# Performance work log

Measured on AMD Instinct MI355X. Metric: run time of the kernel, lower is better.

Reference implementation:

```python
import jax, jax.numpy as jnp
import numpy as np
from jax.scipy.special import logsumexp

ENTROPY_REG = 0.1   # entropy regularization (temperature)
N_ITERS = 100       # Sinkhorn-Knopp iterations (fixed, jit-friendly)


def setup_inputs() -> dict:
    key = jax.random.key(0)
    B, n = 128, 512
    X = jax.random.normal(key, (B, n, n), dtype=jnp.float32)
    return {"X": X}


def _sinkhorn_project(X):
    """Entropy-regularized projection of Q=X onto the doubly-stochastic
    polytope (Birkhoff polytope). This is the hand-written Sinkhorn-Knopp
    replacement for the generic CvxpyLayer conic solve: alternating row/col
    normalization of exp(X / entropy_reg), carried out in log-space for
    numerical stability. Output P satisfies P @ 1 = 1, 1^T P = 1^T, 0<=P<=1.
    """
    logP = X / ENTROPY_REG  # [B, n, n]

    def step(logP, _):
        # row normalization (each row sums to 1)
        logP = logP - logsumexp(logP, axis=-1, keepdims=True)
        # column normalization (each column sums to 1)
        logP = logP - logsumexp(logP, axis=-2, keepdims=True)
        return logP, None

    logP, _ = jax.lax.scan(step, logP, None, length=N_ITERS)
    return jnp.exp(logP)


def reference(X):
    return _sinkhorn_project(X)
```

## Files before the change

### kernel.cpp

```cpp
#include <hip/hip_runtime.h>
#include <math.h>

#define N 512
#define NITERS 100
#define SC 10.0f

__device__ __forceinline__ unsigned int pack_bf16(float a, float b) {
    unsigned int ua = __float_as_uint(a);
    unsigned int ub = __float_as_uint(b);
    ua = (ua + 0x7fffu + ((ua >> 16) & 1u)) >> 16;
    ub = (ub + 0x7fffu + ((ub >> 16) & 1u)) >> 16;
    return ua | (ub << 16);
}

__global__ __launch_bounds__(1024, 1)
void sinkhorn_mult(const float* __restrict__ X, float* __restrict__ P) {
    __shared__ float w_s[N];
    __shared__ float m_s[N];
    __shared__ float lnS_s[N];
    __shared__ float c_lds[16 * N];

    const int tid  = threadIdx.x;
    const int lane = tid & 63;
    const int wave = tid >> 6;

    const size_t base = (size_t)blockIdx.x * N * N;
    const float* __restrict__ A   = X + base;
    float*       __restrict__ out = P + base;
    unsigned short* __restrict__ Kb = (unsigned short*)(P + base);

    if (tid < N) w_s[tid] = 1.0f;

    #pragma unroll 1
    for (int r = wave; r < N; r += 16) {
        const float4* rowp = (const float4*)(A + (size_t)r * N);
        float4 a0 = rowp[lane];
        float4 a1 = rowp[lane + 64];
        float x0 = a0.x * SC, x1 = a0.y * SC, x2 = a0.z * SC, x3 = a0.w * SC;
        float x4 = a1.x * SC, x5 = a1.y * SC, x6 = a1.z * SC, x7 = a1.w * SC;
        float mx = fmaxf(fmaxf(fmaxf(x0, x1), fmaxf(x2, x3)),
                         fmaxf(fmaxf(x4, x5), fmaxf(x6, x7)));
        #pragma unroll
        for (int o = 32; o > 0; o >>= 1) mx = fmaxf(mx, __shfl_xor(mx, o, 64));
        uint2 p0, p1;
        p0.x = pack_bf16(__expf(x0 - mx), __expf(x1 - mx));
        p0.y = pack_bf16(__expf(x2 - mx), __expf(x3 - mx));
        p1.x = pack_bf16(__expf(x4 - mx), __expf(x5 - mx));
        p1.y = pack_bf16(__expf(x6 - mx), __expf(x7 - mx));
        uint2* krow = (uint2*)(Kb + (size_t)r * N);
        krow[lane]      = p0;
        krow[lane + 64] = p1;
        if (lane == 0) m_s[r] = mx;
    }
    __threadfence();
    __syncthreads();

    const size_t RSTEP = (size_t)16 * N;
    for (int it = 0; it < NITERS; ++it) {
        float4 w0 = *(const float4*)(w_s + 8 * lane);
        float4 w1 = *(const float4*)(w_s + 8 * lane + 4);
        float c0 = 0.f, c1 = 0.f, c2 = 0.f, c3 = 0.f,
              c4 = 0.f, c5 = 0.f, c6 = 0.f, c7 = 0.f;
        const bool last = (it == NITERS - 1);

        const unsigned short* kp = Kb + (size_t)wave * N;
        uint4 kq = ((const uint4*)kp)[lane];
        #pragma unroll 1
        for (int r = wave; r < N; r += 16) {
            uint4 nq;
            if (r + 16 < N) nq = ((const uint4*)(kp + RSTEP))[lane];
            float f0 = __uint_as_float(kq.x << 16);
            float f1 = __uint_as_float(kq.x & 0xffff0000u);
            float f2 = __uint_as_float(kq.y << 16);
            float f3 = __uint_as_float(kq.y & 0xffff0000u);
            float f4 = __uint_as_float(kq.z << 16);
            float f5 = __uint_as_float(kq.z & 0xffff0000u);
            float f6 = __uint_as_float(kq.w << 16);
            float f7 = __uint_as_float(kq.w & 0xffff0000u);
            float e0 = f0 * w0.x, e1 = f1 * w0.y, e2 = f2 * w0.z, e3 = f3 * w0.w;
            float e4 = f4 * w1.x, e5 = f5 * w1.y, e6 = f6 * w1.z, e7 = f7 * w1.w;
            float s = ((e0 + e1) + (e2 + e3)) + ((e4 + e5) + (e6 + e7));
            #pragma unroll
            for (int o = 32; o > 0; o >>= 1) s += __shfl_xor(s, o, 64);
            float invS = __builtin_amdgcn_rcpf(s);
            c0 = fmaf(e0, invS, c0); c1 = fmaf(e1, invS, c1);
            c2 = fmaf(e2, invS, c2); c3 = fmaf(e3, invS, c3);
            c4 = fmaf(e4, invS, c4); c5 = fmaf(e5, invS, c5);
            c6 = fmaf(e6, invS, c6); c7 = fmaf(e7, invS, c7);
            if (last && lane == 0) lnS_s[r] = __logf(s);
            kq = nq; kp += RSTEP;
        }

        *(float4*)(c_lds + wave * N + 8 * lane)     = make_float4(c0, c1, c2, c3);
        *(float4*)(c_lds + wave * N + 8 * lane + 4) = make_float4(c4, c5, c6, c7);
        __syncthreads();
        if (tid < N) {
            float cs = 0.f;
            #pragma unroll
            for (int w = 0; w < 16; ++w) cs += c_lds[w * N + tid];
            w_s[tid] = w_s[tid] / fmaxf(cs, 1e-38f);
        }
        __syncthreads();
    }

    float* g_s  = c_lds;
    float* rt_s = c_lds + N;
    if (tid < N) {
        g_s[tid]  = __logf(w_s[tid]);
        rt_s[tid] = -(m_s[tid] + lnS_s[tid]);
    }
    __syncthreads();

    #pragma unroll 1
    for (int r = wave; r < N; r += 16) {
        const float rt = rt_s[r];
        const float4* rowp = (const float4*)(A + (size_t)r * N);
        float4 a0 = rowp[lane];
        float4 a1 = rowp[lane + 64];
        float4 g0 = *(const float4*)(g_s + 4 * lane);
        float4 g1 = *(const float4*)(g_s + 256 + 4 * lane);
        float4 o0, o1;
        o0.x = __expf(fmaf(a0.x, SC, rt) + g0.x);
        o0.y = __expf(fmaf(a0.y, SC, rt) + g0.y);
        o0.z = __expf(fmaf(a0.z, SC, rt) + g0.z);
        o0.w = __expf(fmaf(a0.w, SC, rt) + g0.w);
        o1.x = __expf(fmaf(a1.x, SC, rt) + g1.x);
        o1.y = __expf(fmaf(a1.y, SC, rt) + g1.y);
        o1.z = __expf(fmaf(a1.z, SC, rt) + g1.z);
        o1.w = __expf(fmaf(a1.w, SC, rt) + g1.w);
        float4* outp = (float4*)(out + (size_t)r * N);
        outp[lane]      = o0;
        outp[lane + 64] = o1;
    }
}

extern "C" void kernel_launch(void* const* d_in, const int* in_sizes, int n_in,
                              void* d_out, int out_size, void* d_ws, size_t ws_size,
                              hipStream_t stream) {
    const float* X = (const float*)d_in[0];
    float* P = (float*)d_out;
    const int batch = in_sizes[0] / (N * N);
    hipLaunchKernelGGL(sinkhorn_mult, dim3(batch), dim3(1024), 0, stream, X, P);
}
```

Measured before the change: 2.183 ms.

## Batch eight rows per wave with deep prefetch and simplify column-scale update

Each wave now processes its rows in groups of eight. It holds eight bf16 K rows in registers and prefetches the next eight, and interleaves the eight cross-lane shuffle reductions to raise memory- and instruction-level parallelism. The column accumulation drops the per-element multiply by w: it sums K/s directly and sets the new column scale to 1/t with a hardware reciprocal instead of a division, which is algebraically equivalent. Holding 16 uint4 buffers under a 1024-thread launch bound leaves little register headroom, so spills are a risk.

```diff
diff --git a/kernel.cpp b/kernel.cpp
--- a/kernel.cpp
+++ b/kernel.cpp
@@ -14,7 +14,7 @@
 }
 
 __global__ __launch_bounds__(1024, 1)
-void sinkhorn_mult(const float* __restrict__ X, float* __restrict__ P) {
+void sinkhorn_batch(const float* __restrict__ X, float* __restrict__ P) {
     __shared__ float w_s[N];
     __shared__ float m_s[N];
     __shared__ float lnS_s[N];
@@ -55,50 +55,91 @@
     __threadfence();
     __syncthreads();
 
-    const size_t RSTEP = (size_t)16 * N;
+    const size_t RS = (size_t)16 * N;
     for (int it = 0; it < NITERS; ++it) {
-        float4 w0 = *(const float4*)(w_s + 8 * lane);
-        float4 w1 = *(const float4*)(w_s + 8 * lane + 4);
-        float c0 = 0.f, c1 = 0.f, c2 = 0.f, c3 = 0.f,
-              c4 = 0.f, c5 = 0.f, c6 = 0.f, c7 = 0.f;
         const bool last = (it == NITERS - 1);
+        const float4 w0 = *(const float4*)(w_s + 8 * lane);
+        const float4 w1 = *(const float4*)(w_s + 8 * lane + 4);
+        float t0 = 0.f, t1 = 0.f, t2 = 0.f, t3 = 0.f,
+              t4 = 0.f, t5 = 0.f, t6 = 0.f, t7 = 0.f;
 
         const unsigned short* kp = Kb + (size_t)wave * N;
-        uint4 kq = ((const uint4*)kp)[lane];
-        #pragma unroll 1
-        for (int r = wave; r < N; r += 16) {
-            uint4 nq;
-            if (r + 16 < N) nq = ((const uint4*)(kp + RSTEP))[lane];
-            float f0 = __uint_as_float(kq.x << 16);
-            float f1 = __uint_as_float(kq.x & 0xffff0000u);
-            float f2 = __uint_as_float(kq.y << 16);
-            float f3 = __uint_as_float(kq.y & 0xffff0000u);
-            float f4 = __uint_as_float(kq.z << 16);
-            float f5 = __uint_as_float(kq.z & 0xffff0000u);
-            float f6 = __uint_as_float(kq.w << 16);
-            float f7 = __uint_as_float(kq.w & 0xffff0000u);
-            float e0 = f0 * w0.x, e1 = f1 * w0.y, e2 = f2 * w0.z, e3 = f3 * w0.w;
-            float e4 = f4 * w1.x, e5 = f5 * w1.y, e6 = f6 * w1.z, e7 = f7 * w1.w;
-            float s = ((e0 + e1) + (e2 + e3)) + ((e4 + e5) + (e6 + e7));
+        uint4 cur[8], nxt[8];
+        #pragma unroll
+        for (int k = 0; k < 8; ++k)
+            cur[k] = ((const uint4*)(kp + (size_t)k * RS))[lane];
+
+        #pragma unroll
+        for (int b = 0; b < 4; ++b) {
+            const unsigned short* np = kp + 8 * RS;
+            if (b < 3) {
+                #pragma unroll
+                for (int k = 0; k < 8; ++k)
+                    nxt[k] = ((const uint4*)(np + (size_t)k * RS))[lane];
+            }
+            float s[8];
             #pragma unroll
-            for (int o = 32; o > 0; o >>= 1) s += __shfl_xor(s, o, 64);
-            float invS = __builtin_amdgcn_rcpf(s);
-            c0 = fmaf(e0, invS, c0); c1 = fmaf(e1, invS, c1);
-            c2 = fmaf(e2, invS, c2); c3 = fmaf(e3, invS, c3);
-            c4 = fmaf(e4, invS, c4); c5 = fmaf(e5, invS, c5);
-            c6 = fmaf(e6, invS, c6); c7 = fmaf(e7, invS, c7);
-            if (last && lane == 0) lnS_s[r] = __logf(s);
-            kq = nq; kp += RSTEP;
+            for (int k = 0; k < 8; ++k) {
+                float f0 = __uint_as_float(cur[k].x << 16);
+                float f1 = __uint_as_float(cur[k].x & 0xffff0000u);
+                float f2 = __uint_as_float(cur[k].y << 16);
+                float f3 = __uint_as_float(cur[k].y & 0xffff0000u);
+                float f4 = __uint_as_float(cur[k].z << 16);
+                float f5 = __uint_as_float(cur[k].z & 0xffff0000u);
+                float f6 = __uint_as_float(cur[k].w << 16);
+                float f7 = __uint_as_float(cur[k].w & 0xffff0000u);
+                float sa = f0 * w0.x;
+                sa = fmaf(f2, w0.z, sa);
+                sa = fmaf(f4, w1.x, sa);
+                sa = fmaf(f6, w1.z, sa);
+                float sb = f1 * w0.y;
+                sb = fmaf(f3, w0.w, sb);
+                sb = fmaf(f5, w1.y, sb);
+                sb = fmaf(f7, w1.w, sb);
+                s[k] = sa + sb;
+            }
+            #pragma unroll
+            for (int o = 32; o > 0; o >>= 1) {
+                #pragma unroll
+                for (int k = 0; k < 8; ++k)
+                    s[k] += __shfl_xor(s[k], o, 64);
+            }
+            if (last && lane == 0) {
+                #pragma unroll
+                for (int k = 0; k < 8; ++k)
+                    lnS_s[wave + 16 * (8 * b + k)] = __logf(s[k]);
+            }
+            #pragma unroll
+            for (int k = 0; k < 8; ++k) s[k] = __builtin_amdgcn_rcpf(s[k]);
+            #pragma unroll
+            for (int k = 0; k < 8; ++k) {
+                const float r = s[k];
+                float f0 = __uint_as_float(cur[k].x << 16);
+                float f1 = __uint_as_float(cur[k].x & 0xffff0000u);
+                float f2 = __uint_as_float(cur[k].y << 16);
+                float f3 = __uint_as_float(cur[k].y & 0xffff0000u);
+                float f4 = __uint_as_float(cur[k].z << 16);
+                float f5 = __uint_as_float(cur[k].z & 0xffff0000u);
+                float f6 = __uint_as_float(cur[k].w << 16);
+                float f7 = __uint_as_float(cur[k].w & 0xffff0000u);
+                t0 = fmaf(f0, r, t0); t1 = fmaf(f1, r, t1);
+                t2 = fmaf(f2, r, t2); t3 = fmaf(f3, r, t3);
+                t4 = fmaf(f4, r, t4); t5 = fmaf(f5, r, t5);
+                t6 = fmaf(f6, r, t6); t7 = fmaf(f7, r, t7);
+            }
+            #pragma unroll
+            for (int k = 0; k < 8; ++k) cur[k] = nxt[k];
+            kp = np;
         }
 
-        *(float4*)(c_lds + wave * N + 8 * lane)     = make_float4(c0, c1, c2, c3);
-        *(float4*)(c_lds + wave * N + 8 * lane + 4) = make_float4(c4, c5, c6, c7);
+        *(float4*)(c_lds + wave * N + 8 * lane)     = make_float4(t0, t1, t2, t3);
+        *(float4*)(c_lds + wave * N + 8 * lane + 4) = make_float4(t4, t5, t6, t7);
         __syncthreads();
         if (tid < N) {
             float cs = 0.f;
             #pragma unroll
             for (int w = 0; w < 16; ++w) cs += c_lds[w * N + tid];
-            w_s[tid] = w_s[tid] / fmaxf(cs, 1e-38f);
+            w_s[tid] = __builtin_amdgcn_rcpf(fmaxf(cs, 1e-38f));
         }
         __syncthreads();
     }
@@ -140,5 +181,5 @@
     const float* X = (const float*)d_in[0];
     float* P = (float*)d_out;
     const int batch = in_sizes[0] / (N * N);
-    hipLaunchKernelGGL(sinkhorn_mult, dim3(batch), dim3(1024), 0, stream, X, P);
+    hipLaunchKernelGGL(sinkhorn_batch, dim3(batch), dim3(1024), 0, stream, X, P);
 }
```

Result: slower. 7.840 ms (+259.1%).

## Batch eight-row loads and reductions in Sinkhorn inner loop with deeper prefetch

Applied to the files above, without the earlier changes.

Each iteration's row loop is fully unrolled into four batches of eight rows per wave, with 16 bf16 row loads kept in flight in two register sets. The eight row sums are reduced together with interleaved shuffles, which is meant to hide load latency and the serial shuffle-reduction chain. The column accumulator now sums K/s without the w factor, so the scaling update becomes a plain reciprocal, dropping one multiply per element and a divide. The launch bound is raised to 4 blocks, which caps VGPRs per thread and may force spills of the 32 extra prefetch registers.

```diff
diff --git a/kernel.cpp b/kernel.cpp
--- a/kernel.cpp
+++ b/kernel.cpp
@@ -13,8 +13,82 @@
     return ua | (ub << 16);
 }
 
-__global__ __launch_bounds__(1024, 1)
-void sinkhorn_mult(const float* __restrict__ X, float* __restrict__ P) {
+__device__ __forceinline__ float rowdot(uint4 q, float4 w0, float4 w1) {
+    float f0 = __uint_as_float(q.x << 16);
+    float f1 = __uint_as_float(q.x & 0xffff0000u);
+    float f2 = __uint_as_float(q.y << 16);
+    float f3 = __uint_as_float(q.y & 0xffff0000u);
+    float f4 = __uint_as_float(q.z << 16);
+    float f5 = __uint_as_float(q.z & 0xffff0000u);
+    float f6 = __uint_as_float(q.w << 16);
+    float f7 = __uint_as_float(q.w & 0xffff0000u);
+    float sa = f0 * w0.x;
+    sa = fmaf(f2, w0.z, sa);
+    sa = fmaf(f4, w1.x, sa);
+    sa = fmaf(f6, w1.z, sa);
+    float sb = f1 * w0.y;
+    sb = fmaf(f3, w0.w, sb);
+    sb = fmaf(f5, w1.y, sb);
+    sb = fmaf(f7, w1.w, sb);
+    return sa + sb;
+}
+
+__device__ __forceinline__ void tacc(uint4 q, float r,
+        float& t0, float& t1, float& t2, float& t3,
+        float& t4, float& t5, float& t6, float& t7) {
+    t0 = fmaf(__uint_as_float(q.x << 16),         r, t0);
+    t1 = fmaf(__uint_as_float(q.x & 0xffff0000u), r, t1);
+    t2 = fmaf(__uint_as_float(q.y << 16),         r, t2);
+    t3 = fmaf(__uint_as_float(q.y & 0xffff0000u), r, t3);
+    t4 = fmaf(__uint_as_float(q.z << 16),         r, t4);
+    t5 = fmaf(__uint_as_float(q.z & 0xffff0000u), r, t5);
+    t6 = fmaf(__uint_as_float(q.w << 16),         r, t6);
+    t7 = fmaf(__uint_as_float(q.w & 0xffff0000u), r, t7);
+}
+
+#define LD(p, k) (((const uint4*)((p) + (size_t)(k) * RS))[lane])
+#define PRE8(S, p) \
+    S##0 = LD(p, 0); S##1 = LD(p, 1); S##2 = LD(p, 2); S##3 = LD(p, 3); \
+    S##4 = LD(p, 4); S##5 = LD(p, 5); S##6 = LD(p, 6); S##7 = LD(p, 7);
+
+#define BATCH8(S, bidx) { \
+    float s0 = rowdot(S##0, w0, w1), s1 = rowdot(S##1, w0, w1); \
+    float s2 = rowdot(S##2, w0, w1), s3 = rowdot(S##3, w0, w1); \
+    float s4 = rowdot(S##4, w0, w1), s5 = rowdot(S##5, w0, w1); \
+    float s6 = rowdot(S##6, w0, w1), s7 = rowdot(S##7, w0, w1); \
+    _Pragma("unroll") \
+    for (int o = 32; o > 0; o >>= 1) { \
+        s0 += __shfl_xor(s0, o, 64); s1 += __shfl_xor(s1, o, 64); \
+        s2 += __shfl_xor(s2, o, 64); s3 += __shfl_xor(s3, o, 64); \
+        s4 += __shfl_xor(s4, o, 64); s5 += __shfl_xor(s5, o, 64); \
+        s6 += __shfl_xor(s6, o, 64); s7 += __shfl_xor(s7, o, 64); \
+    } \
+    if (last && lane == 0) { \
+        lnS_s[wave + 16 * (8 * (bidx) + 0)] = __logf(s0); \
+        lnS_s[wave + 16 * (8 * (bidx) + 1)] = __logf(s1); \
+        lnS_s[wave + 16 * (8 * (bidx) + 2)] = __logf(s2); \
+        lnS_s[wave + 16 * (8 * (bidx) + 3)] = __logf(s3); \
+        lnS_s[wave + 16 * (8 * (bidx) + 4)] = __logf(s4); \
+        lnS_s[wave + 16 * (8 * (bidx) + 5)] = __logf(s5); \
+        lnS_s[wave + 16 * (8 * (bidx) + 6)] = __logf(s6); \
+        lnS_s[wave + 16 * (8 * (bidx) + 7)] = __logf(s7); \
+    } \
+    s0 = __builtin_amdgcn_rcpf(s0); s1 = __builtin_amdgcn_rcpf(s1); \
+    s2 = __builtin_amdgcn_rcpf(s2); s3 = __builtin_amdgcn_rcpf(s3); \
+    s4 = __builtin_amdgcn_rcpf(s4); s5 = __builtin_amdgcn_rcpf(s5); \
+    s6 = __builtin_amdgcn_rcpf(s6); s7 = __builtin_amdgcn_rcpf(s7); \
+    tacc(S##0, s0, t0, t1, t2, t3, t4, t5, t6, t7); \
+    tacc(S##1, s1, t0, t1, t2, t3, t4, t5, t6, t7); \
+    tacc(S##2, s2, t0, t1, t2, t3, t4, t5, t6, t7); \
+    tacc(S##3, s3, t0, t1, t2, t3, t4, t5, t6, t7); \
+    tacc(S##4, s4, t0, t1, t2, t3, t4, t5, t6, t7); \
+    tacc(S##5, s5, t0, t1, t2, t3, t4, t5, t6, t7); \
+    tacc(S##6, s6, t0, t1, t2, t3, t4, t5, t6, t7); \
+    tacc(S##7, s7, t0, t1, t2, t3, t4, t5, t6, t7); \
+}
+
+__global__ __launch_bounds__(1024, 4)
+void sinkhorn_ssa(const float* __restrict__ X, float* __restrict__ P) {
     __shared__ float w_s[N];
     __shared__ float m_s[N];
     __shared__ float lnS_s[N];
@@ -55,50 +129,35 @@
     __threadfence();
     __syncthreads();
 
-    const size_t RSTEP = (size_t)16 * N;
+    const size_t RS = (size_t)16 * N;
     for (int it = 0; it < NITERS; ++it) {
-        float4 w0 = *(const float4*)(w_s + 8 * lane);
-        float4 w1 = *(const float4*)(w_s + 8 * lane + 4);
-        float c0 = 0.f, c1 = 0.f, c2 = 0.f, c3 = 0.f,
-              c4 = 0.f, c5 = 0.f, c6 = 0.f, c7 = 0.f;
         const bool last = (it == NITERS - 1);
+        const float4 w0 = *(const float4*)(w_s + 8 * lane);
+        const float4 w1 = *(const float4*)(w_s + 8 * lane + 4);
+        float t0 = 0.f, t1 = 0.f, t2 = 0.f, t3 = 0.f,
+              t4 = 0.f, t5 = 0.f, t6 = 0.f, t7 = 0.f;
 
         const unsigned short* kp = Kb + (size_t)wave * N;
-        uint4 kq = ((const uint4*)kp)[lane];
-        #pragma unroll 1
-        for (int r = wave; r < N; r += 16) {
-            uint4 nq;
-            if (r + 16 < N) nq = ((const uint4*)(kp + RSTEP))[lane];
-            float f0 = __uint_as_float(kq.x << 16);
-            float f1 = __uint_as_float(kq.x & 0xffff0000u);
-            float f2 = __uint_as_float(kq.y << 16);
-            float f3 = __uint_as_float(kq.y & 0xffff0000u);
-            float f4 = __uint_as_float(kq.z << 16);
-            float f5 = __uint_as_float(kq.z & 0xffff0000u);
-            float f6 = __uint_as_float(kq.w << 16);
-            float f7 = __uint_as_float(kq.w & 0xffff0000u);
-            float e0 = f0 * w0.x, e1 = f1 * w0.y, e2 = f2 * w0.z, e3 = f3 * w0.w;
-            float e4 = f4 * w1.x, e5 = f5 * w1.y, e6 = f6 * w1.z, e7 = f7 * w1.w;
-            float s = ((e0 + e1) + (e2 + e3)) + ((e4 + e5) + (e6 + e7));
-            #pragma unroll
-            for (int o = 32; o > 0; o >>= 1) s += __shfl_xor(s, o, 64);
-            float invS = __builtin_amdgcn_rcpf(s);
-            c0 = fmaf(e0, invS, c0); c1 = fmaf(e1, invS, c1);
-            c2 = fmaf(e2, invS, c2); c3 = fmaf(e3, invS, c3);
-            c4 = fmaf(e4, invS, c4); c5 = fmaf(e5, invS, c5);
-            c6 = fmaf(e6, invS, c6); c7 = fmaf(e7, invS, c7);
-            if (last && lane == 0) lnS_s[r] = __logf(s);
-            kq = nq; kp += RSTEP;
-        }
-
-        *(float4*)(c_lds + wave * N + 8 * lane)     = make_float4(c0, c1, c2, c3);
-        *(float4*)(c_lds + wave * N + 8 * lane + 4) = make_float4(c4, c5, c6, c7);
+        uint4 a0, a1, a2, a3, a4, a5, a6, a7;
+        uint4 b0, b1, b2, b3, b4, b5, b6, b7;
+
+        PRE8(a, kp)
+        PRE8(b, kp + 8 * RS)
+        BATCH8(a, 0)
+        PRE8(a, kp + 16 * RS)
+        BATCH8(b, 1)
+        PRE8(b, kp + 24 * RS)
+        BATCH8(a, 2)
+        BATCH8(b, 3)
+
+        *(float4*)(c_lds + wave * N + 8 * lane)     = make_float4(t0, t1, t2, t3);
+        *(float4*)(c_lds + wave * N + 8 * lane + 4) = make_float4(t4, t5, t6, t7);
         __syncthreads();
         if (tid < N) {
             float cs = 0.f;
             #pragma unroll
             for (int w = 0; w < 16; ++w) cs += c_lds[w * N + tid];
-            w_s[tid] = w_s[tid] / fmaxf(cs, 1e-38f);
+            w_s[tid] = __builtin_amdgcn_rcpf(fmaxf(cs, 1e-38f));
         }
         __syncthreads();
     }
@@ -140,5 +199,5 @@
     const float* X = (const float*)d_in[0];
     float* P = (float*)d_out;
     const int batch = in_sizes[0] / (N * N);
-    hipLaunchKernelGGL(sinkhorn_mult, dim3(batch), dim3(1024), 0, stream, X, P);
-}
+    hipLaunchKernelGGL(sinkhorn_ssa, dim3(batch), dim3(1024), 0, stream, X, P);
+}
```

Measured after the change: 7.859 ms. 3.6x slower.

## Store transposed bf16 kernel copy and split iteration into two matvec passes

Applied to the files above, without the earlier changes.

Alongside the row-major bf16 copy of exp(X/eps), the prologue now also builds a transposed bf16 copy through an LDS slab. Each Sinkhorn iteration then runs two plain matvecs, K^T-style for the row sums and K for the column sums, each with FMA accumulation and 4-deep register prefetch. This removes the per-row wave shuffle reduction and the per-row reciprocal that sat inside the inner loop. In exchange, each iteration reads twice as much K data, adds an extra __syncthreads round, and puts a barrier-heavy transpose into the prologue.

```diff
diff --git a/kernel.cpp b/kernel.cpp
--- a/kernel.cpp
+++ b/kernel.cpp
@@ -13,12 +13,21 @@
     return ua | (ub << 16);
 }
 
-__global__ __launch_bounds__(1024, 1)
-void sinkhorn_mult(const float* __restrict__ X, float* __restrict__ P) {
-    __shared__ float w_s[N];
-    __shared__ float m_s[N];
-    __shared__ float lnS_s[N];
+#define UPFMA8(Q, W, z0,z1,z2,z3,z4,z5,z6,z7) \
+    z0 = fmaf(__uint_as_float((Q).x << 16),         (W), z0); \
+    z1 = fmaf(__uint_as_float((Q).x & 0xffff0000u), (W), z1); \
+    z2 = fmaf(__uint_as_float((Q).y << 16),         (W), z2); \
+    z3 = fmaf(__uint_as_float((Q).y & 0xffff0000u), (W), z3); \
+    z4 = fmaf(__uint_as_float((Q).z << 16),         (W), z4); \
+    z5 = fmaf(__uint_as_float((Q).z & 0xffff0000u), (W), z5); \
+    z6 = fmaf(__uint_as_float((Q).w << 16),         (W), z6); \
+    z7 = fmaf(__uint_as_float((Q).w & 0xffff0000u), (W), z7);
+
+__global__ __launch_bounds__(1024)
+void sinkhorn_2layout(const float* __restrict__ X, float* __restrict__ P) {
+    __shared__ float w_s[N], r_s[N], m_s[N], lnS_s[N];
     __shared__ float c_lds[16 * N];
+    __shared__ unsigned int slab_u[16 * 256];
 
     const int tid  = threadIdx.x;
     const int lane = tid & 63;
@@ -27,19 +36,20 @@
     const size_t base = (size_t)blockIdx.x * N * N;
     const float* __restrict__ A   = X + base;
     float*       __restrict__ out = P + base;
-    unsigned short* __restrict__ Kb = (unsigned short*)(P + base);
+    unsigned short* Kb = (unsigned short*)(P + base);
+    unsigned short* Kt = Kb + (size_t)N * N;
 
     if (tid < N) w_s[tid] = 1.0f;
 
-    #pragma unroll 1
-    for (int r = wave; r < N; r += 16) {
+    for (int b = 0; b < 32; ++b) {
+        const int r = 16 * b + wave;
         const float4* rowp = (const float4*)(A + (size_t)r * N);
         float4 a0 = rowp[lane];
         float4 a1 = rowp[lane + 64];
-        float x0 = a0.x * SC, x1 = a0.y * SC, x2 = a0.z * SC, x3 = a0.w * SC;
-        float x4 = a1.x * SC, x5 = a1.y * SC, x6 = a1.z * SC, x7 = a1.w * SC;
-        float mx = fmaxf(fmaxf(fmaxf(x0, x1), fmaxf(x2, x3)),
-                         fmaxf(fmaxf(x4, x5), fmaxf(x6, x7)));
+        float x0 = a0.x*SC, x1 = a0.y*SC, x2 = a0.z*SC, x3 = a0.w*SC;
+        float x4 = a1.x*SC, x5 = a1.y*SC, x6 = a1.z*SC, x7 = a1.w*SC;
+        float mx = fmaxf(fmaxf(fmaxf(x0,x1), fmaxf(x2,x3)),
+                         fmaxf(fmaxf(x4,x5), fmaxf(x6,x7)));
         #pragma unroll
         for (int o = 32; o > 0; o >>= 1) mx = fmaxf(mx, __shfl_xor(mx, o, 64));
         uint2 p0, p1;
@@ -51,54 +61,105 @@
         krow[lane]      = p0;
         krow[lane + 64] = p1;
         if (lane == 0) m_s[r] = mx;
+        *(uint2*)(slab_u + wave * 256 + 2 * lane)       = p0;
+        *(uint2*)(slab_u + wave * 256 + 128 + 2 * lane) = p1;
+        __syncthreads();
+        {
+            const int c = tid >> 1, h = tid & 1;
+            const unsigned short* sl = (const unsigned short*)slab_u;
+            unsigned short v0 = sl[(8*h+0)*N + c];
+            unsigned short v1 = sl[(8*h+1)*N + c];
+            unsigned short v2 = sl[(8*h+2)*N + c];
+            unsigned short v3 = sl[(8*h+3)*N + c];
+            unsigned short v4 = sl[(8*h+4)*N + c];
+            unsigned short v5 = sl[(8*h+5)*N + c];
+            unsigned short v6 = sl[(8*h+6)*N + c];
+            unsigned short v7 = sl[(8*h+7)*N + c];
+            uint4 q;
+            q.x = v0 | ((unsigned)v1 << 16);
+            q.y = v2 | ((unsigned)v3 << 16);
+            q.z = v4 | ((unsigned)v5 << 16);
+            q.w = v6 | ((unsigned)v7 << 16);
+            *(uint4*)(Kt + (size_t)c * N + 16 * b + 8 * h) = q;
+        }
+        __syncthreads();
     }
     __threadfence();
     __syncthreads();
 
-    const size_t RSTEP = (size_t)16 * N;
+    const uint4* KtV = (const uint4*)Kt;
+    const uint4* KbV = (const uint4*)Kb;
+
     for (int it = 0; it < NITERS; ++it) {
-        float4 w0 = *(const float4*)(w_s + 8 * lane);
-        float4 w1 = *(const float4*)(w_s + 8 * lane + 4);
-        float c0 = 0.f, c1 = 0.f, c2 = 0.f, c3 = 0.f,
-              c4 = 0.f, c5 = 0.f, c6 = 0.f, c7 = 0.f;
         const bool last = (it == NITERS - 1);
 
-        const unsigned short* kp = Kb + (size_t)wave * N;
-        uint4 kq = ((const uint4*)kp)[lane];
-        #pragma unroll 1
-        for (int r = wave; r < N; r += 16) {
-            uint4 nq;
-            if (r + 16 < N) nq = ((const uint4*)(kp + RSTEP))[lane];
-            float f0 = __uint_as_float(kq.x << 16);
-            float f1 = __uint_as_float(kq.x & 0xffff0000u);
-            float f2 = __uint_as_float(kq.y << 16);
-            float f3 = __uint_as_float(kq.y & 0xffff0000u);
-            float f4 = __uint_as_float(kq.z << 16);
-            float f5 = __uint_as_float(kq.z & 0xffff0000u);
-            float f6 = __uint_as_float(kq.w << 16);
-            float f7 = __uint_as_float(kq.w & 0xffff0000u);
-            float e0 = f0 * w0.x, e1 = f1 * w0.y, e2 = f2 * w0.z, e3 = f3 * w0.w;
-            float e4 = f4 * w1.x, e5 = f5 * w1.y, e6 = f6 * w1.z, e7 = f7 * w1.w;
-            float s = ((e0 + e1) + (e2 + e3)) + ((e4 + e5) + (e6 + e7));
-            #pragma unroll
-            for (int o = 32; o > 0; o >>= 1) s += __shfl_xor(s, o, 64);
-            float invS = __builtin_amdgcn_rcpf(s);
-            c0 = fmaf(e0, invS, c0); c1 = fmaf(e1, invS, c1);
-            c2 = fmaf(e2, invS, c2); c3 = fmaf(e3, invS, c3);
-            c4 = fmaf(e4, invS, c4); c5 = fmaf(e5, invS, c5);
-            c6 = fmaf(e6, invS, c6); c7 = fmaf(e7, invS, c7);
-            if (last && lane == 0) lnS_s[r] = __logf(s);
-            kq = nq; kp += RSTEP;
-        }
-
-        *(float4*)(c_lds + wave * N + 8 * lane)     = make_float4(c0, c1, c2, c3);
-        *(float4*)(c_lds + wave * N + 8 * lane + 4) = make_float4(c4, c5, c6, c7);
+        {
+            float s0=0.f,s1=0.f,s2=0.f,s3=0.f,s4=0.f,s5=0.f,s6=0.f,s7=0.f;
+            const int J = 32 * wave;
+            const uint4* p = KtV + (size_t)J * 64 + lane;
+            uint4 c0 = p[0], c1 = p[64], c2 = p[128], c3 = p[192];
+            #pragma unroll
+            for (int g = 0; g < 8; ++g) {
+                uint4 n0, n1, n2, n3;
+                if (g < 7) {
+                    const uint4* q = p + (size_t)(g + 1) * 256;
+                    n0 = q[0]; n1 = q[64]; n2 = q[128]; n3 = q[192];
+                }
+                const float wa = w_s[J + 4*g + 0];
+                const float wb = w_s[J + 4*g + 1];
+                const float wc = w_s[J + 4*g + 2];
+                const float wd = w_s[J + 4*g + 3];
+                UPFMA8(c0, wa, s0,s1,s2,s3,s4,s5,s6,s7)
+                UPFMA8(c1, wb, s0,s1,s2,s3,s4,s5,s6,s7)
+                UPFMA8(c2, wc, s0,s1,s2,s3,s4,s5,s6,s7)
+                UPFMA8(c3, wd, s0,s1,s2,s3,s4,s5,s6,s7)
+                if (g < 7) { c0 = n0; c1 = n1; c2 = n2; c3 = n3; }
+            }
+            *(float4*)(c_lds + wave * N + 8 * lane)     = make_float4(s0,s1,s2,s3);
+            *(float4*)(c_lds + wave * N + 8 * lane + 4) = make_float4(s4,s5,s6,s7);
+        }
         __syncthreads();
         if (tid < N) {
             float cs = 0.f;
             #pragma unroll
             for (int w = 0; w < 16; ++w) cs += c_lds[w * N + tid];
-            w_s[tid] = w_s[tid] / fmaxf(cs, 1e-38f);
+            cs = fmaxf(cs, 1e-38f);
+            if (last) lnS_s[tid] = __logf(cs);
+            r_s[tid] = __builtin_amdgcn_rcpf(cs);
+        }
+        __syncthreads();
+
+        {
+            float t0=0.f,t1=0.f,t2=0.f,t3=0.f,t4=0.f,t5=0.f,t6=0.f,t7=0.f;
+            const int I = 32 * wave;
+            const uint4* p = KbV + (size_t)I * 64 + lane;
+            uint4 c0 = p[0], c1 = p[64], c2 = p[128], c3 = p[192];
+            #pragma unroll
+            for (int g = 0; g < 8; ++g) {
+                uint4 n0, n1, n2, n3;
+                if (g < 7) {
+                    const uint4* q = p + (size_t)(g + 1) * 256;
+                    n0 = q[0]; n1 = q[64]; n2 = q[128]; n3 = q[192];
+                }
+                const float ra = r_s[I + 4*g + 0];
+                const float rb = r_s[I + 4*g + 1];
+                const float rc = r_s[I + 4*g + 2];
+                const float rd = r_s[I + 4*g + 3];
+                UPFMA8(c0, ra, t0,t1,t2,t3,t4,t5,t6,t7)
+                UPFMA8(c1, rb, t0,t1,t2,t3,t4,t5,t6,t7)
+                UPFMA8(c2, rc, t0,t1,t2,t3,t4,t5,t6,t7)
+                UPFMA8(c3, rd, t0,t1,t2,t3,t4,t5,t6,t7)
+                if (g < 7) { c0 = n0; c1 = n1; c2 = n2; c3 = n3; }
+            }
+            *(float4*)(c_lds + wave * N + 8 * lane)     = make_float4(t0,t1,t2,t3);
+            *(float4*)(c_lds + wave * N + 8 * lane + 4) = make_float4(t4,t5,t6,t7);
+        }
+        __syncthreads();
+        if (tid < N) {
+            float ct = 0.f;
+            #pragma unroll
+            for (int w = 0; w < 16; ++w) ct += c_lds[w * N + tid];
+            w_s[tid] = __builtin_amdgcn_rcpf(fmaxf(ct, 1e-38f));
         }
         __syncthreads();
     }
@@ -140,5 +201,5 @@
     const float* X = (const float*)d_in[0];
     float* P = (float*)d_out;
     const int batch = in_sizes[0] / (N * N);
-    hipLaunchKernelGGL(sinkhorn_mult, dim3(batch), dim3(1024), 0, stream, X, P);
+    hipLaunchKernelGGL(sinkhorn_2layout, dim3(batch), dim3(1024), 0, stream, X, P);
 }
```

Result: slower. 2.517 ms (+15.3%).
